# Optimization experiments

Hardware: AMD Instinct MI355X
Metric: run time of the kernel (lower is better)

Reference implementation:

```python
import math
import jax, jax.numpy as jnp
import numpy as np

SQ = 2048   # sequence length (hard-coded in source views)
B = 1       # batch (input_[:, 0, :] in QKVLinear)
H = 2048    # HIDDEN_SIZE
NH = 16     # NUM_HEADS
HD = 128    # head dim


def setup_inputs() -> dict:
    key = jax.random.key(0)
    ks = jax.random.split(key, 8)
    hidden_states = jax.random.normal(ks[0], (SQ, B, H), dtype=jnp.float32)
    # causal mask: True = masked (upper triangle, strictly above diagonal)
    attention_mask = jnp.triu(jnp.ones((SQ, SQ), dtype=bool), k=1)[None, None]
    qkv_w = jax.random.normal(ks[1], (3 * H, H), dtype=jnp.float32) * 0.02
    qkv_b = jax.random.normal(ks[2], (3 * H,), dtype=jnp.float32) * 0.02
    # SVD rotation matrices (approximately norm-preserving random matrices)
    svd_token = jax.random.normal(ks[3], (H, H), dtype=jnp.float32) / math.sqrt(H)
    svd_qk = jax.random.normal(ks[4], (NH, HD, HD), dtype=jnp.float32) / math.sqrt(HD)
    svd_vlin = jax.random.normal(ks[5], (NH, HD, HD), dtype=jnp.float32) / math.sqrt(HD)
    dense_w = jax.random.normal(ks[6], (NH, HD, H), dtype=jnp.float32) * 0.02
    dense_b = jax.random.normal(ks[7], (H,), dtype=jnp.float32) * 0.02
    return {
        "hidden_states": hidden_states,
        "attention_mask": attention_mask,
        "qkv_w": qkv_w,
        "qkv_b": qkv_b,
        "svd_token": svd_token,
        "svd_qk": svd_qk,
        "svd_vlin": svd_vlin,
        "dense_w": dense_w,
        "dense_b": dense_b,
    }


def reference(hidden_states, attention_mask, qkv_w, qkv_b, svd_token,
              svd_qk, svd_vlin, dense_w, dense_b):
    # QKVLinear: project input and weight through token-SVD (drop fraction = 0 -> no zeroing)
    x = hidden_states[:, 0, :] @ svd_token                 # [sq, H]
    w = qkv_w @ svd_token                                  # [3H, H]
    mixed = x @ w.T + qkv_b                                # [sq, 3H]
    mixed = mixed.reshape(SQ, B, NH, 3 * HD)
    q, k, v = jnp.split(mixed, 3, axis=-1)                 # each [sq, b, nh, hd]

    # per-head SVD-rotated Q/K (qk_drop = 0 -> h_mask is all-False, no zeroing)
    q = jnp.einsum('sbhd,hde->sbhe', q, svd_qk)
    k = jnp.einsum('sbhd,hde->sbhe', k, svd_qk)

    # scores: baddbmm with alpha = 1/(sqrt(hd)*coeff), then softmax rescales by coeff;
    # with layer_num=1 coeff=1, masked positions end at exactly -10000.
    scale = 1.0 / math.sqrt(HD)
    scores = jnp.einsum('sbhd,tbhd->bhst', q, k) * scale   # [b, nh, sq, sq]
    scores = jnp.where(attention_mask, -10000.0, scores)
    probs = jax.nn.softmax(scores, axis=-1)                # dropout in eval mode (identity)

    # per-head SVD-rotated V (vlinear_drop = 0 -> no zeroing)
    vv = jnp.einsum('sbhd,hde->sbhe', v, svd_vlin)
    ctx = jnp.einsum('bhst,tbhe->sbhe', probs, vv).reshape(SQ, B, H)

    # AttnOutputLinear: tsr block for head h = (dense_w[h].T @ svd_vlin[h]).T = svd_vlin[h].T @ dense_w[h]
    tsr = jnp.einsum('hde,hdo->heo', svd_vlin, dense_w).reshape(H, H)
    out = ctx @ tsr + dense_b                              # [sq, b, H]
    return out
```

## Files before the change

### kernel.cpp

```cpp
#include <hip/hip_runtime.h>
#include <hip/hip_bf16.h>
#include <stdint.h>
#include <math.h>


typedef __bf16 bf16_t;
typedef __bf16 bf16x8 __attribute__((ext_vector_type(8)));
typedef __bf16 bf16x4 __attribute__((ext_vector_type(4)));
typedef float  f32x4  __attribute__((ext_vector_type(4)));

__device__ __forceinline__ void async16(const void* g, void* l) {
  __builtin_amdgcn_global_load_lds(
      (const __attribute__((address_space(1))) void*)(uintptr_t)g,
      (__attribute__((address_space(3))) void*)(uint32_t)(uintptr_t)l,
      16, 0, 0);
}

__global__ __launch_bounds__(256)
void gemm_nt128(const bf16_t* __restrict__ A, const bf16_t* __restrict__ B,
                void* __restrict__ Cv, const void* __restrict__ biasv,
                int K, int lda, int ldb, int ldc, float alpha, int flags)
{
  const int bm0 = blockIdx.y * 128;
  const int bn0 = blockIdx.x * 128;

  __shared__ bf16_t shA[8192];
  __shared__ bf16_t shB[8192];

  const int t  = threadIdx.x;
  const int w  = t >> 6;
  const int l  = t & 63;
  const int wm = (w >> 1) * 64;
  const int wn = (w & 1) * 64;
  const int r0 = l >> 2;
  const int c0 = ((l & 3) ^ ((l >> 3) & 3)) * 8;
  const int fr = l & 15;
  const int kc = l >> 4;
  const int swr = ((fr >> 1) & 3);

  f32x4 acc[4][4];
  #pragma unroll
  for (int i = 0; i < 4; ++i)
    #pragma unroll
    for (int j = 0; j < 4; ++j)
      #pragma unroll
      for (int r = 0; r < 4; ++r)
        acc[i][j][r] = 0.0f;

  for (int k0 = 0; k0 < K; k0 += 64) {
    #pragma unroll
    for (int u = 0; u < 4; ++u) {
      const int seg  = u * 4 + w;
      const int half = seg >> 3;
      const int s8   = seg & 7;
      const int row  = s8 * 16 + r0;
      const int gk   = k0 + half * 32 + c0;
      async16(A + (long long)(bm0 + row) * lda + gk, &shA[half * 4096 + s8 * 512]);
      async16(B + (long long)(bn0 + row) * ldb + gk, &shB[half * 4096 + s8 * 512]);
    }
    __builtin_amdgcn_s_waitcnt(0);
    __syncthreads();

    const int rc = (kc ^ swr) * 8;
    #pragma unroll
    for (int h = 0; h < 2; ++h) {
      bf16x8 af[4], bfv[4];
      #pragma unroll
      for (int i = 0; i < 4; ++i) {
        af[i]  = *(const bf16x8*)&shA[h * 4096 + (wm + i * 16 + fr) * 32 + rc];
        bfv[i] = *(const bf16x8*)&shB[h * 4096 + (wn + i * 16 + fr) * 32 + rc];
      }
      #pragma unroll
      for (int i = 0; i < 4; ++i)
        #pragma unroll
        for (int j = 0; j < 4; ++j)
          acc[i][j] = __builtin_amdgcn_mfma_f32_16x16x32_bf16(af[i], bfv[j], acc[i][j], 0, 0, 0);
    }
    __syncthreads();
  }

  const int cc = l & 15;
  const int rq = (l >> 4) * 4;
  bf16_t* C = (bf16_t*)Cv;
  const bf16_t* bias = (flags & 8) ? (const bf16_t*)biasv : nullptr;
  #pragma unroll
  for (int j = 0; j < 4; ++j) {
    const int col = bn0 + wn + j * 16 + cc;
    const float bv = bias ? (float)bias[col] : 0.0f;
    #pragma unroll
    for (int i = 0; i < 4; ++i)
      #pragma unroll
      for (int r = 0; r < 4; ++r) {
        const int row = bm0 + wm + i * 16 + rq + r;
        C[(long long)row * ldc + col] = (bf16_t)(acc[i][j][r] * alpha + bv);
      }
  }
}

__global__ __launch_bounds__(256)
void gemm_nt64k(const bf16_t* __restrict__ A, const bf16_t* __restrict__ B,
                void* __restrict__ Cv, const void* __restrict__ biasv,
                int K, int lda, int ldb, int ldc, float alpha, int flags)
{
  const int bm0 = blockIdx.y * 64;
  const int bn0 = blockIdx.x * 128;

  __shared__ bf16_t shA[8192];
  __shared__ bf16_t shB[16384];

  const int t  = threadIdx.x;
  const int w  = t >> 6;
  const int l  = t & 63;
  const int wm = (w >> 1) * 32;
  const int wn = (w & 1) * 64;
  const int r0 = l >> 2;
  const int c0 = ((l & 3) ^ ((l >> 3) & 3)) * 8;
  const int fr = l & 15;
  const int kc = l >> 4;
  const int swr = ((fr >> 1) & 3);

  f32x4 acc[2][4];
  #pragma unroll
  for (int i = 0; i < 2; ++i)
    #pragma unroll
    for (int j = 0; j < 4; ++j)
      #pragma unroll
      for (int r = 0; r < 4; ++r)
        acc[i][j][r] = 0.0f;

  for (int k0 = 0; k0 < K; k0 += 128) {
    #pragma unroll
    for (int u = 0; u < 4; ++u) {
      const int seg = u * 4 + w;
      const int q   = seg >> 2;
      const int s4  = seg & 3;
      async16(A + (long long)(bm0 + s4 * 16 + r0) * lda + (k0 + q * 32 + c0),
              &shA[q * 2048 + s4 * 512]);
    }
    #pragma unroll
    for (int u = 0; u < 8; ++u) {
      const int seg = u * 4 + w;
      const int q   = seg >> 3;
      const int s8  = seg & 7;
      async16(B + (long long)(bn0 + s8 * 16 + r0) * ldb + (k0 + q * 32 + c0),
              &shB[q * 4096 + s8 * 512]);
    }
    __builtin_amdgcn_s_waitcnt(0);
    __syncthreads();

    const int rc = (kc ^ swr) * 8;
    #pragma unroll
    for (int q = 0; q < 4; ++q) {
      bf16x8 af[2], bfv[4];
      #pragma unroll
      for (int i = 0; i < 2; ++i)
        af[i]  = *(const bf16x8*)&shA[q * 2048 + (wm + i * 16 + fr) * 32 + rc];
      #pragma unroll
      for (int j = 0; j < 4; ++j)
        bfv[j] = *(const bf16x8*)&shB[q * 4096 + (wn + j * 16 + fr) * 32 + rc];
      #pragma unroll
      for (int i = 0; i < 2; ++i)
        #pragma unroll
        for (int j = 0; j < 4; ++j)
          acc[i][j] = __builtin_amdgcn_mfma_f32_16x16x32_bf16(af[i], bfv[j], acc[i][j], 0, 0, 0);
    }
    __syncthreads();
  }

  const int cc = l & 15;
  const int rq = (l >> 4) * 4;
  if (flags & 4) {
    float* C = (float*)Cv;
    const float* bias = (const float*)biasv;
    #pragma unroll
    for (int j = 0; j < 4; ++j) {
      const int col = bn0 + wn + j * 16 + cc;
      const float bv = bias ? bias[col] : 0.0f;
      #pragma unroll
      for (int i = 0; i < 2; ++i)
        #pragma unroll
        for (int r = 0; r < 4; ++r) {
          const int row = bm0 + wm + i * 16 + rq + r;
          C[(long long)row * ldc + col] = acc[i][j][r] * alpha + bv;
        }
    }
  } else {
    bf16_t* C = (bf16_t*)Cv;
    #pragma unroll
    for (int j = 0; j < 4; ++j) {
      const int col = bn0 + wn + j * 16 + cc;
      #pragma unroll
      for (int i = 0; i < 2; ++i)
        #pragma unroll
        for (int r = 0; r < 4; ++r) {
          const int row = bm0 + wm + i * 16 + rq + r;
          C[(long long)row * ldc + col] = (bf16_t)(acc[i][j][r] * alpha);
        }
    }
  }
}

__global__ __launch_bounds__(256)
void gemm_mprep(const bf16_t* __restrict__ qkT, const bf16_t* __restrict__ vlT,
                const bf16_t* __restrict__ qkv_wT, const bf16_t* __restrict__ dwT,
                bf16_t* __restrict__ Wrot, bf16_t* __restrict__ tsrT,
                const bf16_t* __restrict__ stb, bf16_t* __restrict__ Mbuf)
{
  __shared__ bf16_t smem[16384];
  const int z = blockIdx.x;
  const int t  = threadIdx.x;
  const int w  = t >> 6;
  const int l  = t & 63;
  const int r0 = l >> 2;
  const int c0 = ((l & 3) ^ ((l >> 3) & 3)) * 8;
  const int fr = l & 15;
  const int kc = l >> 4;
  const int swr = ((fr >> 1) & 3);
  const int cc = l & 15;
  const int rq = (l >> 4) * 4;

  if (z < 1024) {
    const int pz = z >> 4, px = z & 15;
    const bf16_t* A;
    const bf16_t* B;
    bf16_t* C;
    int bm0, bn0;
    if (pz < 48) {
      const int h = pz / 3, p = pz - 3 * h;
      A = (p == 2 ? vlT : qkT) + h * 16384;
      B = qkv_wT + (long long)pz * 262144;
      C = Wrot + (long long)pz * 262144;
      bm0 = 0;  bn0 = px * 128;
    } else {
      const int b = pz - 48;
      A = dwT + (long long)b * 262144;
      B = vlT + b * 16384;
      C = tsrT;
      bm0 = px * 128;  bn0 = b * 128;
    }
    bf16_t* shA = smem;
    bf16_t* shB = smem + 8192;
    const int wm = (w >> 1) * 64;
    const int wn = (w & 1) * 64;
    const int arow0 = (pz < 48 ? 0 : bm0);
    const int brow0 = (pz < 48 ? bn0 : 0);

    f32x4 acc[4][4];
    #pragma unroll
    for (int i = 0; i < 4; ++i)
      #pragma unroll
      for (int j = 0; j < 4; ++j)
        #pragma unroll
        for (int r = 0; r < 4; ++r)
          acc[i][j][r] = 0.0f;

    for (int k0 = 0; k0 < 128; k0 += 64) {
      #pragma unroll
      for (int u = 0; u < 4; ++u) {
        const int seg  = u * 4 + w;
        const int half = seg >> 3;
        const int s8   = seg & 7;
        const int row  = s8 * 16 + r0;
        const int gk   = k0 + half * 32 + c0;
        async16(A + (long long)(arow0 + row) * 128 + gk, &shA[half * 4096 + s8 * 512]);
        async16(B + (long long)(brow0 + row) * 128 + gk, &shB[half * 4096 + s8 * 512]);
      }
      __builtin_amdgcn_s_waitcnt(0);
      __syncthreads();

      const int rc = (kc ^ swr) * 8;
      #pragma unroll
      for (int h = 0; h < 2; ++h) {
        bf16x8 af[4], bfv[4];
        #pragma unroll
        for (int i = 0; i < 4; ++i) {
          af[i]  = *(const bf16x8*)&shA[h * 4096 + (wm + i * 16 + fr) * 32 + rc];
          bfv[i] = *(const bf16x8*)&shB[h * 4096 + (wn + i * 16 + fr) * 32 + rc];
        }
        #pragma unroll
        for (int i = 0; i < 4; ++i)
          #pragma unroll
          for (int j = 0; j < 4; ++j)
            acc[i][j] = __builtin_amdgcn_mfma_f32_16x16x32_bf16(af[i], bfv[j], acc[i][j], 0, 0, 0);
      }
      __syncthreads();
    }

    #pragma unroll
    for (int j = 0; j < 4; ++j) {
      const int col = bn0 + wn + j * 16 + cc;
      #pragma unroll
      for (int i = 0; i < 4; ++i)
        #pragma unroll
        for (int r = 0; r < 4; ++r) {
          const int row = arow0 + wm + i * 16 + rq + r;
          C[(long long)row * 2048 + col] = (bf16_t)acc[i][j][r];
        }
    }
  } else {
    const int m = z - 1024;
    const int bm0 = (m >> 4) * 64;
    const int bn0 = (m & 15) * 128;
    bf16_t* shA = smem;
    bf16_t* shB = smem + 4096;
    const int wm = (w >> 1) * 32;
    const int wn = (w & 1) * 64;

    f32x4 acc[2][4];
    #pragma unroll
    for (int i = 0; i < 2; ++i)
      #pragma unroll
      for (int j = 0; j < 4; ++j)
        #pragma unroll
        for (int r = 0; r < 4; ++r)
          acc[i][j][r] = 0.0f;

    for (int k0 = 0; k0 < 2048; k0 += 64) {
      #pragma unroll
      for (int u = 0; u < 2; ++u) {
        const int seg  = u * 4 + w;
        const int half = seg >> 2;
        const int s4   = seg & 3;
        async16(stb + (long long)(bm0 + s4 * 16 + r0) * 2048 + (k0 + half * 32 + c0),
                &shA[half * 2048 + s4 * 512]);
      }
      #pragma unroll
      for (int u = 0; u < 4; ++u) {
        const int seg  = u * 4 + w;
        const int half = seg >> 3;
        const int s8   = seg & 7;
        async16(stb + (long long)(bn0 + s8 * 16 + r0) * 2048 + (k0 + half * 32 + c0),
                &shB[half * 4096 + s8 * 512]);
      }
      __builtin_amdgcn_s_waitcnt(0);
      __syncthreads();

      const int rc = (kc ^ swr) * 8;
      #pragma unroll
      for (int h = 0; h < 2; ++h) {
        bf16x8 af[2], bfv[4];
        #pragma unroll
        for (int i = 0; i < 2; ++i)
          af[i]  = *(const bf16x8*)&shA[h * 2048 + (wm + i * 16 + fr) * 32 + rc];
        #pragma unroll
        for (int j = 0; j < 4; ++j)
          bfv[j] = *(const bf16x8*)&shB[h * 4096 + (wn + j * 16 + fr) * 32 + rc];
        #pragma unroll
        for (int i = 0; i < 2; ++i)
          #pragma unroll
          for (int j = 0; j < 4; ++j)
            acc[i][j] = __builtin_amdgcn_mfma_f32_16x16x32_bf16(af[i], bfv[j], acc[i][j], 0, 0, 0);
      }
      __syncthreads();
    }

    #pragma unroll
    for (int j = 0; j < 4; ++j) {
      const int col = bn0 + wn + j * 16 + cc;
      #pragma unroll
      for (int i = 0; i < 2; ++i)
        #pragma unroll
        for (int r = 0; r < 4; ++r) {
          const int row = bm0 + wm + i * 16 + rq + r;
          Mbuf[(long long)row * 2048 + col] = (bf16_t)acc[i][j][r];
        }
    }
  }
}

__global__ __launch_bounds__(256)
void flash_k(const bf16_t* __restrict__ mixed, const bf16_t* __restrict__ vT,
             bf16_t* __restrict__ ctx, float iscale)
{
  const int h  = blockIdx.x;
  const int qt = 31 - (int)blockIdx.y;
  const int r0g = qt * 64;
  const int niter = (qt >> 1) + 1;
  const bf16_t* Qp = mixed + h * 384;
  const bf16_t* Kp = mixed + h * 384 + 128;
  const bf16_t* Vp = vT + (long long)h * 262144;

  __shared__ bf16_t sKV[128 * 128];
  __shared__ bf16_t sP[64 * 136];
  __shared__ float  sL[2][64];

  const int t  = threadIdx.x;
  const int w  = t >> 6;
  const int l  = t & 63;
  const int wm = (w >> 1) * 32;
  const int wn = (w & 1) * 64;
  const int fr = l & 15;
  const int kc = l >> 4;

  bf16x8 aq[2][4];
  #pragma unroll
  for (int i = 0; i < 2; ++i)
    #pragma unroll
    for (int ks = 0; ks < 4; ++ks)
      aq[i][ks] = *(const bf16x8*)(Qp + (long long)(r0g + wm + i * 16 + fr) * 6144
                                      + ks * 32 + kc * 8);

  f32x4 oacc[2][4];
  #pragma unroll
  for (int i = 0; i < 2; ++i)
    #pragma unroll
    for (int j = 0; j < 4; ++j)
      #pragma unroll
      for (int r = 0; r < 4; ++r) oacc[i][j][r] = 0.0f;
  float lsum[2][4];
  #pragma unroll
  for (int i = 0; i < 2; ++i)
    #pragma unroll
    for (int r = 0; r < 4; ++r) lsum[i][r] = 0.0f;

  for (int it = 0; it < niter; ++it) {
    const int t0 = it * 128;
    #pragma unroll
    for (int s = 0; s < 8; ++s) {
      const int chunk = (w * 8 + s) * 64 + l;
      const int r = chunk >> 4;
      const int c = (chunk & 15) ^ (r & 7);
      async16(Kp + (long long)(t0 + r) * 6144 + c * 8, &sKV[(w * 8 + s) * 512]);
    }
    __builtin_amdgcn_s_waitcnt(0);
    __syncthreads();

    f32x4 acc[2][4];
    #pragma unroll
    for (int i = 0; i < 2; ++i)
      #pragma unroll
      for (int j = 0; j < 4; ++j)
        #pragma unroll
        for (int r = 0; r < 4; ++r) acc[i][j][r] = 0.0f;
    #pragma unroll
    for (int ks = 0; ks < 4; ++ks) {
      bf16x8 bk[4];
      #pragma unroll
      for (int j = 0; j < 4; ++j) {
        const int r = wn + j * 16 + fr;
        const int c = (ks * 4 + kc) ^ (r & 7);
        bk[j] = *(const bf16x8*)&sKV[r * 128 + c * 8];
      }
      #pragma unroll
      for (int i = 0; i < 2; ++i)
        #pragma unroll
        for (int j = 0; j < 4; ++j)
          acc[i][j] = __builtin_amdgcn_mfma_f32_16x16x32_bf16(aq[i][ks], bk[j], acc[i][j], 0, 0, 0);
    }

    #pragma unroll
    for (int i = 0; i < 2; ++i) {
      #pragma unroll
      for (int r = 0; r < 4; ++r) {
        const int rowl = wm + i * 16 + kc * 4 + r;
        const int Rg = r0g + rowl;
        float rs = 0.f;
        #pragma unroll
        for (int j = 0; j < 4; ++j) {
          const int coll = wn + j * 16 + fr;
          const float e = (t0 + coll <= Rg) ? __expf(acc[i][j][r] * iscale) : 0.0f;
          rs += e;
          sP[rowl * 136 + coll] = (bf16_t)e;
        }
        rs += __shfl_xor(rs, 1, 64);
        rs += __shfl_xor(rs, 2, 64);
        rs += __shfl_xor(rs, 4, 64);
        rs += __shfl_xor(rs, 8, 64);
        if (fr == 0) sL[w & 1][rowl] = rs;
      }
    }
    __syncthreads();

    #pragma unroll
    for (int i = 0; i < 2; ++i)
      #pragma unroll
      for (int r = 0; r < 4; ++r) {
        const int rowl = wm + i * 16 + kc * 4 + r;
        lsum[i][r] += sL[0][rowl] + sL[1][rowl];
      }
    #pragma unroll
    for (int s = 0; s < 8; ++s) {
      const int chunk = (w * 8 + s) * 64 + l;
      const int r = chunk >> 4;
      const int c = (chunk & 15) ^ (r & 7);
      async16(Vp + (long long)r * 2048 + t0 + c * 8, &sKV[(w * 8 + s) * 512]);
    }
    __builtin_amdgcn_s_waitcnt(0);
    __syncthreads();

    #pragma unroll
    for (int ks = 0; ks < 4; ++ks) {
      bf16x8 ap[2], bv[4];
      #pragma unroll
      for (int i = 0; i < 2; ++i)
        ap[i] = *(const bf16x8*)&sP[(wm + i * 16 + fr) * 136 + ks * 32 + kc * 8];
      #pragma unroll
      for (int j = 0; j < 4; ++j) {
        const int r = wn + j * 16 + fr;
        const int c = (ks * 4 + kc) ^ (r & 7);
        bv[j] = *(const bf16x8*)&sKV[r * 128 + c * 8];
      }
      #pragma unroll
      for (int i = 0; i < 2; ++i)
        #pragma unroll
        for (int j = 0; j < 4; ++j)
          oacc[i][j] = __builtin_amdgcn_mfma_f32_16x16x32_bf16(ap[i], bv[j], oacc[i][j], 0, 0, 0);
    }
    __syncthreads();
  }

  #pragma unroll
  for (int i = 0; i < 2; ++i) {
    #pragma unroll
    for (int r = 0; r < 4; ++r) {
      const int rowl = wm + i * 16 + kc * 4 + r;
      const float inv = 1.0f / lsum[i][r];
      #pragma unroll
      for (int j = 0; j < 4; ++j) {
        const int coll = wn + j * 16 + fr;
        ctx[(long long)(r0g + rowl) * 2048 + h * 128 + coll] = (bf16_t)(oacc[i][j][r] * inv);
      }
    }
  }
}

__global__ __launch_bounds__(256)
void front_k(const float* __restrict__ hs, bf16_t* __restrict__ hsb,
             const float* __restrict__ svd_tok, bf16_t* __restrict__ stb,
             const float* __restrict__ svd_qk, bf16_t* __restrict__ qkT,
             const float* __restrict__ svd_vl, bf16_t* __restrict__ vlT,
             const float* __restrict__ qkv_w, bf16_t* __restrict__ qkv_wT,
             const float* __restrict__ dense_w, bf16_t* __restrict__ dwT,
             const float* __restrict__ qkv_b, bf16_t* __restrict__ brot)
{
  __shared__ bf16_t sm[32][33];
  const int z = blockIdx.x;
  const int tid = threadIdx.x;

  if (z < 2048) {
    const float* in = (z < 1024) ? hs : svd_tok;
    bf16_t* out = (z < 1024) ? hsb : stb;
    const int base = (z & 1023) * 4096 + tid * 16;
    #pragma unroll
    for (int j = 0; j < 4; ++j) {
      const f32x4 v = *(const f32x4*)(in + base + j * 4);
      bf16x4 o;
      #pragma unroll
      for (int k = 0; k < 4; ++k) o[k] = (bf16_t)v[k];
      *(bf16x4*)(out + base + j * 4) = o;
    }
  } else if (z < 2560) {
    const int zz = z - 2048;
    const int zr = zz >> 4;
    const int tile = zz & 15;
    const float* ip = (zr < 16 ? svd_qk : svd_vl) + (long long)(zr & 15) * 16384;
    bf16_t* op = (zr < 16 ? qkT : vlT) + (long long)(zr & 15) * 16384;
    const int r0 = (tile & 3) << 5;
    const int c0 = (tile >> 2) << 5;
    const int tx = tid & 31;
    const int ty = tid >> 5;
    #pragma unroll
    for (int yy = ty; yy < 32; yy += 8)
      sm[yy][tx] = (bf16_t)ip[(long long)(r0 + yy) * 128 + c0 + tx];
    __syncthreads();
    #pragma unroll
    for (int yy = ty; yy < 32; yy += 8)
      op[(long long)(c0 + yy) * 128 + r0 + tx] = sm[tx][yy];
  } else if (z < 18944) {
    const int zz = z - 2560;
    const int zb = zz >> 8;
    const int tile = zz & 255;
    const float* ip = (zb < 48) ? qkv_w + (long long)zb * 262144
                                : dense_w + (long long)(zb - 48) * 262144;
    bf16_t* op = (zb < 48) ? qkv_wT + (long long)zb * 262144
                           : dwT + (long long)(zb - 48) * 262144;
    const int r0 = (tile & 3) << 5;
    const int c0 = (tile >> 2) << 5;
    const int tx = tid & 31;
    const int ty = tid >> 5;
    #pragma unroll
    for (int yy = ty; yy < 32; yy += 8)
      sm[yy][tx] = (bf16_t)ip[(long long)(r0 + yy) * 2048 + c0 + tx];
    __syncthreads();
    #pragma unroll
    for (int yy = ty; yy < 32; yy += 8)
      op[(long long)(c0 + yy) * 128 + r0 + tx] = sm[tx][yy];
  } else {
    const int hp = (z - 18944) * 2 + (tid >> 7);
    const int h = hp / 3, p = hp % 3;
    const int e = tid & 127;
    const float* R = (p == 2 ? (const float*)svd_vl : (const float*)svd_qk) + (long long)h * 16384;
    const float* b = qkv_b + h * 384 + p * 128;
    float acc = 0.f;
    for (int d = 0; d < 128; ++d)
      acc += b[d] * R[d * 128 + e];
    brot[h * 384 + p * 128 + e] = (bf16_t)acc;
  }
}

__global__ __launch_bounds__(256)
void transpose_b2b(const bf16_t* __restrict__ in, bf16_t* __restrict__ out,
                   int R, long long zsi, int rsi, long long zso)
{
  __shared__ bf16_t sm[32][33];
  const int z  = blockIdx.z;
  const int r0 = blockIdx.x << 5;
  const int c0 = blockIdx.y << 5;
  const int tx = threadIdx.x & 31;
  const int ty = threadIdx.x >> 5;
  const bf16_t* ip = in + (long long)z * zsi;
  bf16_t* op = out + (long long)z * zso;
  #pragma unroll
  for (int yy = ty; yy < 32; yy += 8)
    sm[yy][tx] = ip[(long long)(r0 + yy) * rsi + c0 + tx];
  __syncthreads();
  #pragma unroll
  for (int yy = ty; yy < 32; yy += 8)
    op[(long long)(c0 + yy) * R + r0 + tx] = sm[tx][yy];
}

extern "C" void kernel_launch(void* const* d_in, const int* in_sizes, int n_in,
                              void* d_out, int out_size, void* d_ws, size_t ws_size,
                              hipStream_t stream)
{
  const float* hs      = (const float*)d_in[0];
  const float* qkv_w   = (const float*)d_in[2];
  const float* qkv_b   = (const float*)d_in[3];
  const float* svd_tok = (const float*)d_in[4];
  const float* svd_qk  = (const float*)d_in[5];
  const float* svd_vl  = (const float*)d_in[6];
  const float* dense_w = (const float*)d_in[7];
  const float* dense_b = (const float*)d_in[8];
  float* out = (float*)d_out;
  bf16_t* ws = (bf16_t*)d_ws;

  bf16_t* hsb    = ws;
  bf16_t* stb    = ws +  4194304LL;
  bf16_t* Mbuf   = ws +  8388608LL;
  bf16_t* x2     = ws + 12582912LL;
  bf16_t* qkv_wT = ws + 16777216LL;
  bf16_t* Wrot   = ws + 29360128LL;
  bf16_t* mixed  = ws + 41943040LL;
  bf16_t* vT     = ws + 54525952LL;
  bf16_t* ctx    = ws + 58720256LL;
  bf16_t* dwT    = ws + 62914560LL;
  bf16_t* tsrT   = ws + 67108864LL;
  bf16_t* qkT    = ws + 71303168LL;
  bf16_t* vlT    = ws + 71565312LL;
  bf16_t* brot   = ws + 71827456LL;
  if (ws_size < 71833600ULL * 2ULL) return;

  const float iscale = 0.08838834764831845f;

  front_k<<<dim3(18968), 256, 0, stream>>>(hs, hsb, svd_tok, stb,
      svd_qk, qkT, svd_vl, vlT, qkv_w, qkv_wT, dense_w, dwT, qkv_b, brot);
  gemm_mprep<<<dim3(1536), 256, 0, stream>>>(qkT, vlT, qkv_wT, dwT,
      Wrot, tsrT, stb, Mbuf);
  gemm_nt64k<<<dim3(16, 32), 256, 0, stream>>>(hsb, Mbuf, x2, nullptr,
      2048, 2048, 2048, 2048, 1.0f, 0);
  gemm_nt128<<<dim3(48, 16), 256, 0, stream>>>(x2, Wrot, mixed, brot,
      2048, 2048, 2048, 6144, 1.0f, 8);
  transpose_b2b<<<dim3(64, 4, 16), 256, 0, stream>>>(mixed + 256, vT, 2048, 384, 6144, 262144);
  flash_k<<<dim3(16, 32), 256, 0, stream>>>(mixed, vT, ctx, iscale);
  gemm_nt64k<<<dim3(16, 32), 256, 0, stream>>>(ctx, tsrT, out, dense_b,
      2048, 2048, 2048, 2048, 1.0f, 4);
}
```

Before: 386.2 us.

## Double-buffer K/V in flash kernel and give each wave full row ownership

The flash attention kernel now keeps separate LDS buffers for K and V. The next K or V tile is prefetched with partial vmcnt waits while the current tile's MFMAs run, instead of loading K then V serially into one buffer with full waits. Each wave now owns 16 query rows across all 128 key columns, so row sums reduce within the wave and the sL shared-memory exchange and a barrier are gone. The change also swizzles the P buffer, raises MFMA priority with setprio, and interleaves heavy and light causal tiles across blockIdx.y to balance load. It uses more LDS per block, which may lower occupancy.

```diff
diff --git a/kernel.cpp b/kernel.cpp
--- a/kernel.cpp
+++ b/kernel.cpp
@@ -368,159 +368,146 @@
   }
 }
 
+__device__ __forceinline__ void stage128(const bf16_t* __restrict__ gp, bf16_t* lds,
+                                         const long long rstride, const int w, const int l)
+{
+  #pragma unroll
+  for (int s = 0; s < 8; ++s) {
+    const int chunk = (w * 8 + s) * 64 + l;
+    const int r = chunk >> 4;
+    const int c = (chunk & 15) ^ (r & 7);
+    async16(gp + (long long)r * rstride + c * 8, &lds[(w * 8 + s) * 512]);
+  }
+}
+
+#define FK_WAIT8() do { asm volatile("s_waitcnt vmcnt(8)" ::: "memory"); \
+                        __builtin_amdgcn_sched_barrier(0); } while (0)
+#define FK_WAIT0() do { asm volatile("s_waitcnt vmcnt(0)" ::: "memory"); \
+                        __builtin_amdgcn_sched_barrier(0); } while (0)
+#define FK_BAR()   do { __builtin_amdgcn_s_barrier(); \
+                        __builtin_amdgcn_sched_barrier(0); } while (0)
+
 __global__ __launch_bounds__(256)
 void flash_k(const bf16_t* __restrict__ mixed, const bf16_t* __restrict__ vT,
              bf16_t* __restrict__ ctx, float iscale)
 {
   const int h  = blockIdx.x;
-  const int qt = 31 - (int)blockIdx.y;
+  const int y  = blockIdx.y;
+  const int qt = (y < 16) ? (31 - y) : (y - 16);
   const int r0g = qt * 64;
   const int niter = (qt >> 1) + 1;
   const bf16_t* Qp = mixed + h * 384;
   const bf16_t* Kp = mixed + h * 384 + 128;
   const bf16_t* Vp = vT + (long long)h * 262144;
 
-  __shared__ bf16_t sKV[128 * 128];
-  __shared__ bf16_t sP[64 * 136];
-  __shared__ float  sL[2][64];
+  __shared__ bf16_t sK[16384];
+  __shared__ bf16_t sV[16384];
+  __shared__ bf16_t sP[8192];
 
   const int t  = threadIdx.x;
   const int w  = t >> 6;
   const int l  = t & 63;
-  const int wm = (w >> 1) * 32;
-  const int wn = (w & 1) * 64;
   const int fr = l & 15;
   const int kc = l >> 4;
-
-  bf16x8 aq[2][4];
-  #pragma unroll
-  for (int i = 0; i < 2; ++i)
-    #pragma unroll
-    for (int ks = 0; ks < 4; ++ks)
-      aq[i][ks] = *(const bf16x8*)(Qp + (long long)(r0g + wm + i * 16 + fr) * 6144
-                                      + ks * 32 + kc * 8);
-
-  f32x4 oacc[2][4];
-  #pragma unroll
-  for (int i = 0; i < 2; ++i)
-    #pragma unroll
-    for (int j = 0; j < 4; ++j)
-      #pragma unroll
-      for (int r = 0; r < 4; ++r) oacc[i][j][r] = 0.0f;
-  float lsum[2][4];
-  #pragma unroll
-  for (int i = 0; i < 2; ++i)
-    #pragma unroll
-    for (int r = 0; r < 4; ++r) lsum[i][r] = 0.0f;
+  const int qrow0 = r0g + w * 16;
+
+  bf16x8 aq[4];
+  #pragma unroll
+  for (int ks = 0; ks < 4; ++ks)
+    aq[ks] = *(const bf16x8*)(Qp + (long long)(qrow0 + fr) * 6144 + ks * 32 + kc * 8);
+
+  f32x4 oacc[8];
+  #pragma unroll
+  for (int j = 0; j < 8; ++j)
+    #pragma unroll
+    for (int r = 0; r < 4; ++r) oacc[j][r] = 0.0f;
+  float lsum[4] = {0.f, 0.f, 0.f, 0.f};
+
+  FK_WAIT0();
+
+  stage128(Kp, sK, 6144, w, l);
+  stage128(Vp, sV, 2048, w, l);
+  FK_WAIT8();
+  FK_BAR();
 
   for (int it = 0; it < niter; ++it) {
     const int t0 = it * 128;
-    #pragma unroll
-    for (int s = 0; s < 8; ++s) {
-      const int chunk = (w * 8 + s) * 64 + l;
-      const int r = chunk >> 4;
-      const int c = (chunk & 15) ^ (r & 7);
-      async16(Kp + (long long)(t0 + r) * 6144 + c * 8, &sKV[(w * 8 + s) * 512]);
-    }
-    __builtin_amdgcn_s_waitcnt(0);
-    __syncthreads();
-
-    f32x4 acc[2][4];
-    #pragma unroll
-    for (int i = 0; i < 2; ++i)
-      #pragma unroll
-      for (int j = 0; j < 4; ++j)
-        #pragma unroll
-        for (int r = 0; r < 4; ++r) acc[i][j][r] = 0.0f;
+
+    f32x4 acc[8];
+    #pragma unroll
+    for (int j = 0; j < 8; ++j)
+      #pragma unroll
+      for (int r = 0; r < 4; ++r) acc[j][r] = 0.0f;
     #pragma unroll
     for (int ks = 0; ks < 4; ++ks) {
-      bf16x8 bk[4];
-      #pragma unroll
-      for (int j = 0; j < 4; ++j) {
-        const int r = wn + j * 16 + fr;
-        const int c = (ks * 4 + kc) ^ (r & 7);
-        bk[j] = *(const bf16x8*)&sKV[r * 128 + c * 8];
-      }
-      #pragma unroll
-      for (int i = 0; i < 2; ++i)
-        #pragma unroll
-        for (int j = 0; j < 4; ++j)
-          acc[i][j] = __builtin_amdgcn_mfma_f32_16x16x32_bf16(aq[i][ks], bk[j], acc[i][j], 0, 0, 0);
-    }
-
-    #pragma unroll
-    for (int i = 0; i < 2; ++i) {
-      #pragma unroll
-      for (int r = 0; r < 4; ++r) {
-        const int rowl = wm + i * 16 + kc * 4 + r;
-        const int Rg = r0g + rowl;
-        float rs = 0.f;
-        #pragma unroll
-        for (int j = 0; j < 4; ++j) {
-          const int coll = wn + j * 16 + fr;
-          const float e = (t0 + coll <= Rg) ? __expf(acc[i][j][r] * iscale) : 0.0f;
-          rs += e;
-          sP[rowl * 136 + coll] = (bf16_t)e;
-        }
-        rs += __shfl_xor(rs, 1, 64);
-        rs += __shfl_xor(rs, 2, 64);
-        rs += __shfl_xor(rs, 4, 64);
-        rs += __shfl_xor(rs, 8, 64);
-        if (fr == 0) sL[w & 1][rowl] = rs;
-      }
-    }
-    __syncthreads();
-
-    #pragma unroll
-    for (int i = 0; i < 2; ++i)
-      #pragma unroll
-      for (int r = 0; r < 4; ++r) {
-        const int rowl = wm + i * 16 + kc * 4 + r;
-        lsum[i][r] += sL[0][rowl] + sL[1][rowl];
-      }
-    #pragma unroll
-    for (int s = 0; s < 8; ++s) {
-      const int chunk = (w * 8 + s) * 64 + l;
-      const int r = chunk >> 4;
-      const int c = (chunk & 15) ^ (r & 7);
-      async16(Vp + (long long)r * 2048 + t0 + c * 8, &sKV[(w * 8 + s) * 512]);
-    }
-    __builtin_amdgcn_s_waitcnt(0);
-    __syncthreads();
+      bf16x8 bk[8];
+      #pragma unroll
+      for (int j = 0; j < 8; ++j)
+        bk[j] = *(const bf16x8*)&sK[(j * 16 + fr) * 128 + (((ks * 4 + kc) ^ (fr & 7)) * 8)];
+      __builtin_amdgcn_s_setprio(1);
+      #pragma unroll
+      for (int j = 0; j < 8; ++j)
+        acc[j] = __builtin_amdgcn_mfma_f32_16x16x32_bf16(aq[ks], bk[j], acc[j], 0, 0, 0);
+      __builtin_amdgcn_s_setprio(0);
+    }
+
+    #pragma unroll
+    for (int r = 0; r < 4; ++r) {
+      const int q16 = kc * 4 + r;
+      const int Rg  = qrow0 + q16;
+      float rs = 0.f;
+      #pragma unroll
+      for (int j = 0; j < 8; ++j) {
+        const float e = (t0 + j * 16 + fr <= Rg) ? __expf(acc[j][r] * iscale) : 0.0f;
+        rs += e;
+        sP[(w * 16 + q16) * 128 + (((j * 2 + (fr >> 3)) ^ (q16 & 7)) * 8) + (fr & 7)] = (bf16_t)e;
+      }
+      rs += __shfl_xor(rs, 1, 64);
+      rs += __shfl_xor(rs, 2, 64);
+      rs += __shfl_xor(rs, 4, 64);
+      rs += __shfl_xor(rs, 8, 64);
+      lsum[r] += rs;
+    }
+
+    FK_BAR();
+    if (it + 1 < niter) {
+      stage128(Kp + (long long)(t0 + 128) * 6144, sK, 6144, w, l);
+      FK_WAIT8();
+    } else {
+      FK_WAIT0();
+    }
+    FK_BAR();
 
     #pragma unroll
     for (int ks = 0; ks < 4; ++ks) {
-      bf16x8 ap[2], bv[4];
-      #pragma unroll
-      for (int i = 0; i < 2; ++i)
-        ap[i] = *(const bf16x8*)&sP[(wm + i * 16 + fr) * 136 + ks * 32 + kc * 8];
-      #pragma unroll
-      for (int j = 0; j < 4; ++j) {
-        const int r = wn + j * 16 + fr;
-        const int c = (ks * 4 + kc) ^ (r & 7);
-        bv[j] = *(const bf16x8*)&sKV[r * 128 + c * 8];
-      }
-      #pragma unroll
-      for (int i = 0; i < 2; ++i)
-        #pragma unroll
-        for (int j = 0; j < 4; ++j)
-          oacc[i][j] = __builtin_amdgcn_mfma_f32_16x16x32_bf16(ap[i], bv[j], oacc[i][j], 0, 0, 0);
-    }
-    __syncthreads();
-  }
-
-  #pragma unroll
-  for (int i = 0; i < 2; ++i) {
-    #pragma unroll
-    for (int r = 0; r < 4; ++r) {
-      const int rowl = wm + i * 16 + kc * 4 + r;
-      const float inv = 1.0f / lsum[i][r];
-      #pragma unroll
-      for (int j = 0; j < 4; ++j) {
-        const int coll = wn + j * 16 + fr;
-        ctx[(long long)(r0g + rowl) * 2048 + h * 128 + coll] = (bf16_t)(oacc[i][j][r] * inv);
-      }
-    }
+      const bf16x8 ap =
+          *(const bf16x8*)&sP[(w * 16 + fr) * 128 + (((ks * 4 + kc) ^ (fr & 7)) * 8)];
+      bf16x8 bv[8];
+      #pragma unroll
+      for (int j = 0; j < 8; ++j)
+        bv[j] = *(const bf16x8*)&sV[(j * 16 + fr) * 128 + (((ks * 4 + kc) ^ (fr & 7)) * 8)];
+      __builtin_amdgcn_s_setprio(1);
+      #pragma unroll
+      for (int j = 0; j < 8; ++j)
+        oacc[j] = __builtin_amdgcn_mfma_f32_16x16x32_bf16(ap, bv[j], oacc[j], 0, 0, 0);
+      __builtin_amdgcn_s_setprio(0);
+    }
+
+    if (it + 1 < niter) {
+      FK_BAR();
+      stage128(Vp + (t0 + 128), sV, 2048, w, l);
+      FK_WAIT8();
+      FK_BAR();
+    }
+  }
+
+  #pragma unroll
+  for (int r = 0; r < 4; ++r) {
+    const float inv = 1.0f / lsum[r];
+    const int rowg = qrow0 + kc * 4 + r;
+    #pragma unroll
+    for (int j = 0; j < 8; ++j)
+      ctx[(long long)rowg * 2048 + h * 128 + j * 16 + fr] = (bf16_t)(oacc[j][r] * inv);
   }
 }
 
```

Measured after the change: 376.2 us. -2.6%, faster.
